# Performance work log

Measured on AMD Instinct MI355X. Metric: run time of the kernel, lower is better.

The kernel has to match this reference:

```python
import jax, jax.numpy as jnp
import numpy as np

N = 8192      # atoms
F = 133       # atom feature length
H = 256       # hidden_size
MF = 200      # mol feature length
RH = 512      # readout_hidden_size
DEPTH = 3
N_RO = 2      # readout_num_hidden_layers
DEG = 32      # avg degree of random graph


def setup_inputs() -> dict:
    key = jax.random.key(0)
    ks = jax.random.split(key, 16)
    sc = 0.05
    adjacency_matrix = (jax.random.uniform(ks[0], (N, N)) < (DEG / N)).astype(jnp.float32)
    atom_feature_matrix = jax.random.normal(ks[1], (N, F), jnp.float32)
    molecule_features_vector = jax.random.normal(ks[2], (MF,), jnp.float32)
    return {
        "adjacency_matrix": adjacency_matrix,
        "atom_feature_matrix": atom_feature_matrix,
        "molecule_features_vector": molecule_features_vector,
        "W_in": jax.random.normal(ks[3], (F, H), jnp.float32) * sc,
        "b_in": jnp.zeros((H,), jnp.float32),
        "W_att": jax.random.normal(ks[4], (2 * H,), jnp.float32) * sc,
        "b_att": jnp.zeros((), jnp.float32),
        "W_node": jax.random.normal(ks[5], (DEPTH, H, H), jnp.float32) * sc,
        "b_node": jnp.zeros((DEPTH, H), jnp.float32),
        "W_ro_in": jax.random.normal(ks[6], (H + MF, RH), jnp.float32) * sc,
        "b_ro_in": jnp.zeros((RH,), jnp.float32),
        "W_ro_hid": jax.random.normal(ks[7], (N_RO, RH, RH), jnp.float32) * sc,
        "b_ro_hid": jnp.zeros((N_RO, RH), jnp.float32),
        "W_out": jax.random.normal(ks[8], (RH,), jnp.float32) * sc,
        "b_out": jnp.zeros((), jnp.float32),
    }


def reference(adjacency_matrix, atom_feature_matrix, molecule_features_vector,
              W_in, b_in, W_att, b_att, W_node, b_node,
              W_ro_in, b_ro_in, W_ro_hid, b_ro_hid, W_out, b_out):
    # input node-level linear
    h = atom_feature_matrix @ W_in + b_in                     # [N, H]
    wa_nei, wa_self = W_att[:H], W_att[H:]                    # concat([neighbor, self]) ordering
    for d in range(DEPTH):
        # attention score[i, j] = sigmoid(w_nei . h_j + w_self . h_i + b)
        s_nei = h @ wa_nei                                    # [N]
        s_self = h @ wa_self                                  # [N]
        att = jax.nn.sigmoid(s_self[:, None] + s_nei[None, :] + b_att)  # [N, N]
        # adjacency is binary: zeros stay zero, nonzeros get scaled by sigmoid score
        h = (adjacency_matrix * att) @ h                      # sum aggregation, [N, H]
        h = jax.nn.relu(h @ W_node[d] + b_node[d])
    # readout: sum over atoms, concat mol features
    g = jnp.sum(h, axis=0)                                    # [H]
    g = jnp.concatenate([g, molecule_features_vector])        # [H + MF]
    g = jax.nn.relu(g @ W_ro_in + b_ro_in)
    for d in range(N_RO):
        g = jax.nn.relu(g @ W_ro_hid[d] + b_ro_hid[d])
    return g @ W_out + b_out                                  # scalar
```

## Files before the change

### kernel.cpp

```cpp
#include <hip/hip_runtime.h>
#include <hip/hip_bf16.h>
#include <math.h>

#define N 8192
#define F 133
#define FP 136
#define H 256
#define MF 200
#define RH 512
#define MAXDEG 128

typedef unsigned short bfu;

static __device__ __forceinline__ bfu f2bf(float f) {
    unsigned u = __builtin_bit_cast(unsigned, f);
    u = (u + 0x7fff + ((u >> 16) & 1)) >> 16;
    return (bfu)u;
}
static __device__ __forceinline__ float bf2f(bfu b) {
    unsigned u = (unsigned)b << 16;
    return __builtin_bit_cast(float, u);
}

__global__ __launch_bounds__(256) void k_front(
    const float4* __restrict__ A4, int* __restrict__ cnt, int* __restrict__ colidx,
    const float* __restrict__ X, const float* __restrict__ Win,
    const float* __restrict__ bin, const float* __restrict__ Watt,
    bfu* __restrict__ hb, float* __restrict__ snei, float* __restrict__ sself,
    float* __restrict__ zbuf) {
    const int t = threadIdx.x;
    const int b = blockIdx.x;
    if (b == 2304) {
        for (int i = t; i < 1800; i += 256) zbuf[i] = 0.f;
        return;
    }
    if (b >= 256) {
        const int lane = t & 63;
        const int row = (b - 256) * 4 + (t >> 6);
        const float4* rowp = A4 + (size_t)row * (N / 4);
        unsigned w4[4];
#pragma unroll 1
        for (int c = 0; c < 4; ++c) {
            float4 v[8];
#pragma unroll
            for (int j = 0; j < 8; ++j) v[j] = rowp[c * 512 + j * 64 + lane];
            unsigned m = 0;
#pragma unroll
            for (int j = 0; j < 8; ++j) {
                const float* vp = &v[j].x;
#pragma unroll
                for (int q = 0; q < 4; ++q)
                    m |= (vp[q] != 0.0f) ? (1u << (j * 4 + q)) : 0u;
            }
            w4[c] = m;
        }
        int tl = __popc(w4[0]) + __popc(w4[1]) + __popc(w4[2]) + __popc(w4[3]);
        int inc = tl;
#pragma unroll
        for (int d = 1; d < 64; d <<= 1) {
            int nb = __shfl_up(inc, d);
            if (lane >= d) inc += nb;
        }
        int o = inc - tl;
        if (lane == 63) cnt[row] = inc < MAXDEG ? inc : MAXDEG;
        int* rowout = colidx + row * MAXDEG;
#pragma unroll
        for (int c = 0; c < 4; ++c) {
            unsigned m = w4[c];
            const int base = c * 2048 + lane * 4;
            while (m) {
                int p = __ffs(m) - 1;
                m &= m - 1;
                if (o < MAXDEG) rowout[o] = base + ((p >> 2) << 8) + (p & 3);
                ++o;
            }
        }
        return;
    }
    __shared__ float xs[32][FP];
    __shared__ float sredN[32][4];
    __shared__ float sredS[32][4];
    const int row0 = b * 32;
    for (int i = t; i < 32 * F; i += 256) {
        int r = i / F, f = i - r * F;
        xs[r][f] = X[(row0 + r) * F + f];
    }
    __syncthreads();
    float acc[32];
#pragma unroll
    for (int r = 0; r < 32; ++r) acc[r] = 0.f;
    for (int f = 0; f < 132; f += 4) {
        float w0 = Win[(f + 0) * H + t];
        float w1 = Win[(f + 1) * H + t];
        float w2 = Win[(f + 2) * H + t];
        float w3 = Win[(f + 3) * H + t];
#pragma unroll
        for (int r = 0; r < 32; ++r) {
            float4 xv = *reinterpret_cast<const float4*>(&xs[r][f]);
            acc[r] = fmaf(xv.x, w0, acc[r]);
            acc[r] = fmaf(xv.y, w1, acc[r]);
            acc[r] = fmaf(xv.z, w2, acc[r]);
            acc[r] = fmaf(xv.w, w3, acc[r]);
        }
    }
    {
        float w0 = Win[132 * H + t];
#pragma unroll
        for (int r = 0; r < 32; ++r) acc[r] = fmaf(xs[r][132], w0, acc[r]);
    }
    const float bb = bin[t];
    const float wan = Watt[t];
    const float was = Watt[H + t];
    const int wv = t >> 6, ln = t & 63;
#pragma unroll
    for (int r = 0; r < 32; ++r) {
        float v = acc[r] + bb;
        hb[(row0 + r) * H + t] = f2bf(v);
        float pn = v * wan;
        float ps = v * was;
        for (int off = 32; off > 0; off >>= 1) {
            pn += __shfl_down(pn, off);
            ps += __shfl_down(ps, off);
        }
        if (ln == 0) { sredN[r][wv] = pn; sredS[r][wv] = ps; }
    }
    __syncthreads();
    if (t < 32)
        snei[row0 + t] = (sredN[t][0] + sredN[t][1]) + (sredN[t][2] + sredN[t][3]);
    else if (t < 64) {
        int r = t - 32;
        sself[row0 + r] = (sredS[r][0] + sredS[r][1]) + (sredS[r][2] + sredS[r][3]);
    }
}

template <bool LAST>
__global__ __launch_bounds__(512, 6) void k_depth(
    const bfu* __restrict__ hin, bfu* __restrict__ hout,
    const int* __restrict__ cnt, const int* __restrict__ colidx,
    const float* __restrict__ snei_in, const float* __restrict__ sself_in,
    float* __restrict__ snei_out, float* __restrict__ sself_out,
    const float* __restrict__ Wn, const float* __restrict__ bn,
    const float* __restrict__ Watt, const float* __restrict__ b_att,
    float* __restrict__ gsum) {
    __shared__ bfu   hsb[32][264];
    __shared__ float uni[4096];
    __shared__ float sred[8 * 256];
    __shared__ float sselfL[32];
    __shared__ int   ncnt[32];
    const int t = threadIdx.x;
    const int w = t >> 6, l = t & 63;
    const int c0 = l << 2;
    const int R0 = blockIdx.x * 32;
    bfu* wlsb = (bfu*)uni;
    unsigned short* jls = ((unsigned short*)uni) + 4096;

    if (t < 32) { ncnt[t] = cnt[R0 + t]; sselfL[t] = sself_in[R0 + t] + b_att[0]; }
    __syncthreads();
#pragma unroll
    for (int rep = 0; rep < 8; ++rep) {
        int idx = t + rep * 512;
        int r = idx >> 7, k = idx & 127;
        if (k < ncnt[r]) {
            int j = colidx[(R0 + r) * MAXDEG + k];
            jls[idx] = (unsigned short)j;
            wlsb[idx] = f2bf(1.f / (1.f + __expf(-(sselfL[r] + snei_in[j]))));
        }
    }
    __syncthreads();
#define GSTEP(u, sx, sy, sz, sw)                                                  \
    { int ju = (int)jls[r * 128 + k + u]; float wv = bf2f(wlsb[r * 128 + k + u]); \
      ushort4 hv = *reinterpret_cast<const ushort4*>(&hin[ju * 256 + c0]);        \
      sx = fmaf(wv, bf2f(hv.x), sx); sy = fmaf(wv, bf2f(hv.y), sy);               \
      sz = fmaf(wv, bf2f(hv.z), sz); sw = fmaf(wv, bf2f(hv.w), sw); }
#pragma unroll 1
    for (int rr = 0; rr < 4; ++rr) {
        const int r = w * 4 + rr;
        const int n = ncnt[r];
        float x0=0,y0=0,z0=0,w0=0, x1=0,y1=0,z1=0,w1=0;
        float x2=0,y2=0,z2=0,w2=0, x3=0,y3=0,z3=0,w3=0;
        float x4=0,y4=0,z4=0,w4=0, x5=0,y5=0,z5=0,w5=0;
        float x6=0,y6=0,z6=0,w6=0, x7=0,y7=0,z7=0,w7=0;
        int k = 0;
        for (; k + 8 <= n; k += 8) {
            GSTEP(0,x0,y0,z0,w0) GSTEP(1,x1,y1,z1,w1)
            GSTEP(2,x2,y2,z2,w2) GSTEP(3,x3,y3,z3,w3)
            GSTEP(4,x4,y4,z4,w4) GSTEP(5,x5,y5,z5,w5)
            GSTEP(6,x6,y6,z6,w6) GSTEP(7,x7,y7,z7,w7)
        }
        for (; k < n; ++k) { GSTEP(0,x0,y0,z0,w0) }
        ushort4 st;
        st.x = f2bf(((x0+x1)+(x2+x3)) + ((x4+x5)+(x6+x7)));
        st.y = f2bf(((y0+y1)+(y2+y3)) + ((y4+y5)+(y6+y7)));
        st.z = f2bf(((z0+z1)+(z2+z3)) + ((z4+z5)+(z6+z7)));
        st.w = f2bf(((w0+w1)+(w2+w3)) + ((w4+w5)+(w6+w7)));
        *reinterpret_cast<ushort4*>(&hsb[r][c0]) = st;
    }
#undef GSTEP
    __syncthreads();

    float* Ws = uni;
    float acc[4][4];
#pragma unroll
    for (int i = 0; i < 4; ++i)
#pragma unroll
        for (int j = 0; j < 4; ++j) acc[i][j] = 0.f;
#pragma unroll 1
    for (int k0 = 0; k0 < 16; ++k0) {
        if (k0) __syncthreads();
#pragma unroll
        for (int j = 0; j < 2; ++j) {
            int idx = j * 512 + t;
            int kr = idx >> 6;
            int nc = (idx & 63) << 2;
            *reinterpret_cast<float4*>(&Ws[kr * 256 + nc]) =
                *reinterpret_cast<const float4*>(&Wn[(k0 * 16 + kr) * 256 + nc]);
        }
        __syncthreads();
#pragma unroll
        for (int k4 = 0; k4 < 4; ++k4) {
            ushort4 a0 = *reinterpret_cast<const ushort4*>(&hsb[w * 4 + 0][k0 * 16 + k4 * 4]);
            ushort4 a1 = *reinterpret_cast<const ushort4*>(&hsb[w * 4 + 1][k0 * 16 + k4 * 4]);
            ushort4 a2 = *reinterpret_cast<const ushort4*>(&hsb[w * 4 + 2][k0 * 16 + k4 * 4]);
            ushort4 a3 = *reinterpret_cast<const ushort4*>(&hsb[w * 4 + 3][k0 * 16 + k4 * 4]);
            float p0[4] = {bf2f(a0.x), bf2f(a0.y), bf2f(a0.z), bf2f(a0.w)};
            float p1[4] = {bf2f(a1.x), bf2f(a1.y), bf2f(a1.z), bf2f(a1.w)};
            float p2[4] = {bf2f(a2.x), bf2f(a2.y), bf2f(a2.z), bf2f(a2.w)};
            float p3[4] = {bf2f(a3.x), bf2f(a3.y), bf2f(a3.z), bf2f(a3.w)};
#pragma unroll
            for (int ki = 0; ki < 4; ++ki) {
                float4 wv = *reinterpret_cast<const float4*>(&Ws[(k4 * 4 + ki) * 256 + c0]);
                float aa0 = p0[ki], aa1 = p1[ki], aa2 = p2[ki], aa3 = p3[ki];
                acc[0][0] = fmaf(aa0, wv.x, acc[0][0]); acc[0][1] = fmaf(aa0, wv.y, acc[0][1]);
                acc[0][2] = fmaf(aa0, wv.z, acc[0][2]); acc[0][3] = fmaf(aa0, wv.w, acc[0][3]);
                acc[1][0] = fmaf(aa1, wv.x, acc[1][0]); acc[1][1] = fmaf(aa1, wv.y, acc[1][1]);
                acc[1][2] = fmaf(aa1, wv.z, acc[1][2]); acc[1][3] = fmaf(aa1, wv.w, acc[1][3]);
                acc[2][0] = fmaf(aa2, wv.x, acc[2][0]); acc[2][1] = fmaf(aa2, wv.y, acc[2][1]);
                acc[2][2] = fmaf(aa2, wv.z, acc[2][2]); acc[2][3] = fmaf(aa2, wv.w, acc[2][3]);
                acc[3][0] = fmaf(aa3, wv.x, acc[3][0]); acc[3][1] = fmaf(aa3, wv.y, acc[3][1]);
                acc[3][2] = fmaf(aa3, wv.z, acc[3][2]); acc[3][3] = fmaf(aa3, wv.w, acc[3][3]);
            }
        }
    }

    const float4 bv = *reinterpret_cast<const float4*>(&bn[c0]);
    float4 wanv, wasv;
    if (!LAST) {
        wanv = *reinterpret_cast<const float4*>(&Watt[c0]);
        wasv = *reinterpret_cast<const float4*>(&Watt[H + c0]);
    }
    float cs[4] = {0.f, 0.f, 0.f, 0.f};
#pragma unroll
    for (int i = 0; i < 4; ++i) {
        float v0 = acc[i][0] + bv.x; v0 = v0 > 0.f ? v0 : 0.f;
        float v1 = acc[i][1] + bv.y; v1 = v1 > 0.f ? v1 : 0.f;
        float v2 = acc[i][2] + bv.z; v2 = v2 > 0.f ? v2 : 0.f;
        float v3 = acc[i][3] + bv.w; v3 = v3 > 0.f ? v3 : 0.f;
        if (!LAST) {
            ushort4 o; o.x = f2bf(v0); o.y = f2bf(v1); o.z = f2bf(v2); o.w = f2bf(v3);
            *reinterpret_cast<ushort4*>(&hout[(R0 + w * 4 + i) * H + c0]) = o;
            float pn = v0 * wanv.x + v1 * wanv.y + v2 * wanv.z + v3 * wanv.w;
            float ps = v0 * wasv.x + v1 * wasv.y + v2 * wasv.z + v3 * wasv.w;
#pragma unroll
            for (int off = 32; off > 0; off >>= 1) {
                pn += __shfl_xor(pn, off);
                ps += __shfl_xor(ps, off);
            }
            if (l == 0) {
                snei_out[R0 + w * 4 + i] = pn;
                sself_out[R0 + w * 4 + i] = ps;
            }
        } else {
            cs[0] += v0; cs[1] += v1; cs[2] += v2; cs[3] += v3;
        }
    }
    if (LAST) {
#pragma unroll
        for (int j = 0; j < 4; ++j) sred[w * 256 + c0 + j] = cs[j];
        __syncthreads();
        if (t < 256) {
            float s = 0.f;
#pragma unroll
            for (int q = 0; q < 8; ++q) s += sred[q * 256 + t];
            atomicAdd(&gsum[t], s);
        }
    }
}

template <int MODE>
__global__ __launch_bounds__(256) void k_t(const float* __restrict__ xsrc,
                                           const float* __restrict__ bp,
                                           const float* __restrict__ mol,
                                           const float* __restrict__ W,
                                           float* __restrict__ pout) {
    const int K = (MODE == 0) ? (H + MF) : RH;
    const int KW = K / 8;
    const int lo = blockIdx.y * KW;
    __shared__ float xin[64];
    __shared__ float red[256];
    const int t = threadIdx.x;
    if (t < KW) {
        int k = lo + t;
        float xv;
        if (MODE == 0) xv = (k < H) ? xsrc[k] : mol[k - H];
        else {
            float p = xsrc[k] + bp[k];
            xv = p > 0.f ? p : 0.f;
        }
        xin[t] = xv;
    }
    __syncthreads();
    const int o = blockIdx.x * 64 + (t & 63);
    const int kg = t >> 6;
    float acc = 0.f;
    for (int k = kg; k < KW; k += 4)
        acc = fmaf(xin[k], W[(lo + k) * RH + o], acc);
    red[t] = acc;
    __syncthreads();
    if (t < 64) {
        float s = red[t] + red[t + 64] + red[t + 128] + red[t + 192];
        atomicAdd(&pout[o], s);
    }
}

__global__ __launch_bounds__(256) void k_t_fin(const float* __restrict__ xsrc,
                                               const float* __restrict__ bp,
                                               const float* __restrict__ W,
                                               float* __restrict__ pout,
                                               const float* __restrict__ b3,
                                               const float* __restrict__ Wo,
                                               const float* __restrict__ bo,
                                               int* __restrict__ done,
                                               float* __restrict__ out) {
    const int KW = RH / 8;
    const int lo = blockIdx.y * KW;
    __shared__ float xin[64];
    __shared__ float red[256];
    __shared__ int lastb;
    const int t = threadIdx.x;
    if (t < KW) {
        float p = xsrc[lo + t] + bp[lo + t];
        xin[t] = p > 0.f ? p : 0.f;
    }
    __syncthreads();
    const int o = blockIdx.x * 64 + (t & 63);
    const int kg = t >> 6;
    float acc = 0.f;
    for (int k = kg; k < KW; k += 4)
        acc = fmaf(xin[k], W[(lo + k) * RH + o], acc);
    red[t] = acc;
    __syncthreads();
    if (t < 64) {
        float s = red[t] + red[t + 64] + red[t + 128] + red[t + 192];
        atomicAdd(&pout[o], s);
    }
    __threadfence();
    __syncthreads();
    if (t == 0) lastb = (atomicAdd(done, 1) == 63) ? 1 : 0;
    __syncthreads();
    if (!lastb) return;
    float v0 = atomicAdd(&pout[t], 0.f) + b3[t];
    float v1 = atomicAdd(&pout[t + 256], 0.f) + b3[t + 256];
    v0 = v0 > 0.f ? v0 : 0.f;
    v1 = v1 > 0.f ? v1 : 0.f;
    red[t] = v0 * Wo[t] + v1 * Wo[t + 256];
    __syncthreads();
    for (int s = 128; s > 0; s >>= 1) {
        if (t < s) red[t] += red[t + s];
        __syncthreads();
    }
    if (t == 0) out[0] = red[0] + bo[0];
}

extern "C" void kernel_launch(void* const* d_in, const int* in_sizes, int n_in,
                              void* d_out, int out_size, void* d_ws, size_t ws_size,
                              hipStream_t stream) {
    const float* A        = (const float*)d_in[0];
    const float* X        = (const float*)d_in[1];
    const float* mol      = (const float*)d_in[2];
    const float* W_in     = (const float*)d_in[3];
    const float* b_in     = (const float*)d_in[4];
    const float* W_att    = (const float*)d_in[5];
    const float* b_att    = (const float*)d_in[6];
    const float* W_node   = (const float*)d_in[7];
    const float* b_node   = (const float*)d_in[8];
    const float* W_ro_in  = (const float*)d_in[9];
    const float* b_ro_in  = (const float*)d_in[10];
    const float* W_ro_hid = (const float*)d_in[11];
    const float* b_ro_hid = (const float*)d_in[12];
    const float* W_out    = (const float*)d_in[13];
    const float* b_out    = (const float*)d_in[14];

    char* ws = (char*)d_ws;
    bfu*   hb_a   = (bfu*)  (ws);
    bfu*   hb_b   = (bfu*)  (ws + 4194304);
    int*   colidx = (int*)  (ws + 8388608);
    int*   cnt    = (int*)  (ws + 12582912);
    float* s0n    = (float*)(ws + 12615680);
    float* s0s    = (float*)(ws + 12648448);
    float* s1n    = (float*)(ws + 12681216);
    float* s1s    = (float*)(ws + 12713984);
    float* zbuf   = (float*)(ws + 12746752);
    float* gsum   = zbuf;
    float* g1p    = zbuf + 256;
    float* g2p    = zbuf + 768;
    float* g3p    = zbuf + 1280;
    int*   done   = (int*)(zbuf + 1792);

    k_front<<<2305, 256, 0, stream>>>((const float4*)A, cnt, colidx,
                                      X, W_in, b_in, W_att, hb_a, s0n, s0s, zbuf);
    k_depth<false><<<256, 512, 0, stream>>>(
        hb_a, hb_b, cnt, colidx, s0n, s0s, s1n, s1s,
        W_node + 0 * H * H, b_node + 0 * H, W_att, b_att, nullptr);
    k_depth<false><<<256, 512, 0, stream>>>(
        hb_b, hb_a, cnt, colidx, s1n, s1s, s0n, s0s,
        W_node + 1 * H * H, b_node + 1 * H, W_att, b_att, nullptr);
    k_depth<true><<<256, 512, 0, stream>>>(
        hb_a, nullptr, cnt, colidx, s0n, s0s, nullptr, nullptr,
        W_node + 2 * H * H, b_node + 2 * H, W_att, b_att, gsum);
    k_t<0><<<dim3(8, 8), 256, 0, stream>>>(gsum, nullptr, mol, W_ro_in, g1p);
    k_t<1><<<dim3(8, 8), 256, 0, stream>>>(g1p, b_ro_in, nullptr, W_ro_hid, g2p);
    k_t_fin<<<dim3(8, 8), 256, 0, stream>>>(g2p, b_ro_hid, W_ro_hid + RH * RH, g3p,
                                            b_ro_hid + RH, W_out, b_out, done,
                                            (float*)d_out);
}
```

Measured before the change: 233.9 us.

## Keep aggregated rows and attention weights in fp32 LDS, double W tile depth

```diff
diff --git a/kernel.cpp b/kernel.cpp
--- a/kernel.cpp
+++ b/kernel.cpp
@@ -134,7 +134,7 @@
 }
 
 template <bool LAST>
-__global__ __launch_bounds__(512, 6) void k_depth(
+__global__ __launch_bounds__(512, 2) void k_depth(
     const bfu* __restrict__ hin, bfu* __restrict__ hout,
     const int* __restrict__ cnt, const int* __restrict__ colidx,
     const float* __restrict__ snei_in, const float* __restrict__ sself_in,
@@ -142,8 +142,8 @@
     const float* __restrict__ Wn, const float* __restrict__ bn,
     const float* __restrict__ Watt, const float* __restrict__ b_att,
     float* __restrict__ gsum) {
-    __shared__ bfu   hsb[32][264];
-    __shared__ float uni[4096];
+    __shared__ float hs[32][260];
+    __shared__ float uni[8192];
     __shared__ float sred[8 * 256];
     __shared__ float sselfL[32];
     __shared__ int   ncnt[32];
@@ -151,8 +151,8 @@
     const int w = t >> 6, l = t & 63;
     const int c0 = l << 2;
     const int R0 = blockIdx.x * 32;
-    bfu* wlsb = (bfu*)uni;
-    unsigned short* jls = ((unsigned short*)uni) + 4096;
+    float* wls = uni;
+    unsigned short* jls = (unsigned short*)(uni + 4096);
 
     if (t < 32) { ncnt[t] = cnt[R0 + t]; sselfL[t] = sself_in[R0 + t] + b_att[0]; }
     __syncthreads();
@@ -163,12 +163,12 @@
         if (k < ncnt[r]) {
             int j = colidx[(R0 + r) * MAXDEG + k];
             jls[idx] = (unsigned short)j;
-            wlsb[idx] = f2bf(1.f / (1.f + __expf(-(sselfL[r] + snei_in[j]))));
+            wls[idx] = 1.f / (1.f + __expf(-(sselfL[r] + snei_in[j])));
         }
     }
     __syncthreads();
 #define GSTEP(u, sx, sy, sz, sw)                                                  \
-    { int ju = (int)jls[r * 128 + k + u]; float wv = bf2f(wlsb[r * 128 + k + u]); \
+    { int ju = (int)jls[r * 128 + k + u]; float wv = wls[r * 128 + k + u];        \
       ushort4 hv = *reinterpret_cast<const ushort4*>(&hin[ju * 256 + c0]);        \
       sx = fmaf(wv, bf2f(hv.x), sx); sy = fmaf(wv, bf2f(hv.y), sy);               \
       sz = fmaf(wv, bf2f(hv.z), sz); sw = fmaf(wv, bf2f(hv.w), sw); }
@@ -188,12 +188,12 @@
             GSTEP(6,x6,y6,z6,w6) GSTEP(7,x7,y7,z7,w7)
         }
         for (; k < n; ++k) { GSTEP(0,x0,y0,z0,w0) }
-        ushort4 st;
-        st.x = f2bf(((x0+x1)+(x2+x3)) + ((x4+x5)+(x6+x7)));
-        st.y = f2bf(((y0+y1)+(y2+y3)) + ((y4+y5)+(y6+y7)));
-        st.z = f2bf(((z0+z1)+(z2+z3)) + ((z4+z5)+(z6+z7)));
-        st.w = f2bf(((w0+w1)+(w2+w3)) + ((w4+w5)+(w6+w7)));
-        *reinterpret_cast<ushort4*>(&hsb[r][c0]) = st;
+        float4 st;
+        st.x = ((x0+x1)+(x2+x3)) + ((x4+x5)+(x6+x7));
+        st.y = ((y0+y1)+(y2+y3)) + ((y4+y5)+(y6+y7));
+        st.z = ((z0+z1)+(z2+z3)) + ((z4+z5)+(z6+z7));
+        st.w = ((w0+w1)+(w2+w3)) + ((w4+w5)+(w6+w7));
+        *reinterpret_cast<float4*>(&hs[r][c0]) = st;
     }
 #undef GSTEP
     __syncthreads();
@@ -205,27 +205,27 @@
 #pragma unroll
         for (int j = 0; j < 4; ++j) acc[i][j] = 0.f;
 #pragma unroll 1
-    for (int k0 = 0; k0 < 16; ++k0) {
+    for (int k0 = 0; k0 < 8; ++k0) {
         if (k0) __syncthreads();
 #pragma unroll
-        for (int j = 0; j < 2; ++j) {
+        for (int j = 0; j < 4; ++j) {
             int idx = j * 512 + t;
             int kr = idx >> 6;
             int nc = (idx & 63) << 2;
             *reinterpret_cast<float4*>(&Ws[kr * 256 + nc]) =
-                *reinterpret_cast<const float4*>(&Wn[(k0 * 16 + kr) * 256 + nc]);
+                *reinterpret_cast<const float4*>(&Wn[(k0 * 32 + kr) * 256 + nc]);
         }
         __syncthreads();
 #pragma unroll
-        for (int k4 = 0; k4 < 4; ++k4) {
-            ushort4 a0 = *reinterpret_cast<const ushort4*>(&hsb[w * 4 + 0][k0 * 16 + k4 * 4]);
-            ushort4 a1 = *reinterpret_cast<const ushort4*>(&hsb[w * 4 + 1][k0 * 16 + k4 * 4]);
-            ushort4 a2 = *reinterpret_cast<const ushort4*>(&hsb[w * 4 + 2][k0 * 16 + k4 * 4]);
-            ushort4 a3 = *reinterpret_cast<const ushort4*>(&hsb[w * 4 + 3][k0 * 16 + k4 * 4]);
-            float p0[4] = {bf2f(a0.x), bf2f(a0.y), bf2f(a0.z), bf2f(a0.w)};
-            float p1[4] = {bf2f(a1.x), bf2f(a1.y), bf2f(a1.z), bf2f(a1.w)};
-            float p2[4] = {bf2f(a2.x), bf2f(a2.y), bf2f(a2.z), bf2f(a2.w)};
-            float p3[4] = {bf2f(a3.x), bf2f(a3.y), bf2f(a3.z), bf2f(a3.w)};
+        for (int k4 = 0; k4 < 8; ++k4) {
+            float4 a0 = *reinterpret_cast<const float4*>(&hs[w * 4 + 0][k0 * 32 + k4 * 4]);
+            float4 a1 = *reinterpret_cast<const float4*>(&hs[w * 4 + 1][k0 * 32 + k4 * 4]);
+            float4 a2 = *reinterpret_cast<const float4*>(&hs[w * 4 + 2][k0 * 32 + k4 * 4]);
+            float4 a3 = *reinterpret_cast<const float4*>(&hs[w * 4 + 3][k0 * 32 + k4 * 4]);
+            const float* p0 = &a0.x;
+            const float* p1 = &a1.x;
+            const float* p2 = &a2.x;
+            const float* p3 = &a3.x;
 #pragma unroll
             for (int ki = 0; ki < 4; ++ki) {
                 float4 wv = *reinterpret_cast<const float4*>(&Ws[(k4 * 4 + ki) * 256 + c0]);
```

Result: faster. 211.0 us, median of 2 (-9.8%).
